# Performance work log

Hardware: AMD Instinct MI355X
Metric: run time of the kernel (lower is better)

The kernel has to match this reference:

```python
import jax, jax.numpy as jnp
import numpy as np

B, T, D, H, L, O = 256, 256, 512, 512, 3, 256
EPS = 1e-5


def setup_inputs() -> dict:
    key = jax.random.key(0)
    ks = jax.random.split(key, 8)
    rn = lambda i, shape, scale=1.0: jax.random.normal(ks[i], shape, dtype=jnp.float32) * scale
    z = lambda *shape: jnp.zeros(shape, jnp.float32)
    o = lambda *shape: jnp.ones(shape, jnp.float32)
    return {
        "x": rn(0, (B, T, D)),
        # layer 0 (non-middle) cell
        "W0": rn(1, (H, D), 0.02), "b0": z(H), "u0": rn(2, (H,)),
        "g1_0": o(H), "be1_0": z(H), "g2_0": o(H), "be2_0": z(H),
        # shared middle cell (layers 1..L-1 share one parameter set)
        "Wm": rn(3, (H, H), 0.02), "bm": z(H), "um": rn(4, (H,)),
        "g1_m": o(H), "be1_m": z(H), "g2_m": o(H), "be2_m": z(H),
        # output head
        "Wfc": rn(5, (O, H), 0.02), "bfc": z(O),
        "batchSize": B,
    }


def _bn(zx, g, b):
    # BatchNorm1d, training mode: batch stats over axis 0, biased variance
    m = jnp.mean(zx, axis=0)
    v = jnp.mean((zx - m) ** 2, axis=0)
    return (zx - m) * jax.lax.rsqrt(v + EPS) * g + b


def _cell(inp, h, W, bb, u, g1, be1, g2, be2):
    out = _bn(inp @ W.T + bb, g1, be1)
    out = jax.nn.relu(out + h * u)  # u is diagonal -> elementwise scale
    return _bn(out, g2, be2)


def reference(x, W0, b0, u0, g1_0, be1_0, g2_0, be2_0,
              Wm, bm, um, g1_m, be1_m, g2_m, be2_m, Wfc, bfc, batchSize):
    nmid = L - 1

    def step(carry, x_t):
        h0, hm = carry  # h0: [B,H], hm: [L-1,B,H]
        h0n = _cell(x_t, h0, W0, b0, u0, g1_0, be1_0, g2_0, be2_0)
        cur = h0n
        new = []
        for j in range(nmid):  # middle layers share params, distinct states
            hj = _cell(cur, hm[j], Wm, bm, um, g1_m, be1_m, g2_m, be2_m)
            new.append(hj)
            cur = hj
        return (h0n, jnp.stack(new)), None

    init = (jnp.zeros((batchSize, H), x.dtype),
            jnp.zeros((nmid, batchSize, H), x.dtype))
    (h0f, hmf), _ = jax.lax.scan(step, init, jnp.swapaxes(x, 0, 1))
    logits = hmf[-1] @ Wfc.T + bfc
    return jax.nn.log_softmax(logits, axis=-1)
```

## Files before the change

### kernel.cpp

```cpp
#include <hip/hip_runtime.h>
#include <math.h>

#define kT 256
#define kEPS 1e-5f
#define NBB 96
#define BT 1024
#define SSTEP 8
#define NT (kT / SSTEP)

typedef __attribute__((ext_vector_type(8))) _Float16 half8;
typedef __attribute__((ext_vector_type(4))) float f32x4;

#define BSLOT(p, j) (((p)*4 + (j)) * 16)
#define BARBYTES (260 * 4 * 64)

__device__ __forceinline__ unsigned packhl(float f) {
    _Float16 hi = (_Float16)f;
    _Float16 lo = (_Float16)(f - (float)hi);
    unsigned short uh, ul;
    __builtin_memcpy(&uh, &hi, 2);
    __builtin_memcpy(&ul, &lo, 2);
    return (unsigned)uh | ((unsigned)ul << 16);
}

__device__ __forceinline__ float unpackhl(unsigned wd) {
    unsigned short uh = (unsigned short)wd, ul = (unsigned short)(wd >> 16);
    _Float16 hi, lo;
    __builtin_memcpy(&hi, &uh, 2);
    __builtin_memcpy(&lo, &ul, 2);
    return (float)hi + (float)lo;
}

__device__ __forceinline__ void split32(uint4 A, uint4 B, half8& hi, half8& lo) {
    unsigned hh[4], ll[4];
    hh[0] = __builtin_amdgcn_perm(A.y, A.x, 0x05040100u);
    ll[0] = __builtin_amdgcn_perm(A.y, A.x, 0x07060302u);
    hh[1] = __builtin_amdgcn_perm(A.w, A.z, 0x05040100u);
    ll[1] = __builtin_amdgcn_perm(A.w, A.z, 0x07060302u);
    hh[2] = __builtin_amdgcn_perm(B.y, B.x, 0x05040100u);
    ll[2] = __builtin_amdgcn_perm(B.y, B.x, 0x07060302u);
    hh[3] = __builtin_amdgcn_perm(B.w, B.z, 0x05040100u);
    ll[3] = __builtin_amdgcn_perm(B.w, B.z, 0x07060302u);
    __builtin_memcpy(&hi, hh, 16);
    __builtin_memcpy(&lo, ll, 16);
}

__global__ __launch_bounds__(256) void w0pack(const float* __restrict__ W0,
                                              unsigned* __restrict__ W0p) {
    const int i4 = (blockIdx.x * 256 + threadIdx.x) * 4;
    float4 v = *(const float4*)(W0 + i4);
    uint4 pw;
    pw.x = packhl(v.x); pw.y = packhl(v.y); pw.z = packhl(v.z); pw.w = packhl(v.w);
    *(uint4*)(W0p + i4) = pw;
}

#define ZROWS 32
#define XSTR 516
__global__ __launch_bounds__(1024, 4) void zgemm(float* __restrict__ x,
                                                 const unsigned* __restrict__ W0p) {
    __shared__ unsigned xs[ZROWS * XSTR];
    const int tid = threadIdx.x;
    const long long r0 = (long long)blockIdx.x * ZROWS;

    {
        const int row = tid >> 5;
        const int k0 = (tid & 31) * 16;
        const float* src = x + (r0 + row) * 512 + k0;
        unsigned* dst = xs + row * XSTR + k0;
#pragma unroll
        for (int i = 0; i < 4; ++i) {
            float4 v = *(const float4*)(src + i * 4);
            uint4 pw;
            pw.x = packhl(v.x); pw.y = packhl(v.y); pw.z = packhl(v.z); pw.w = packhl(v.w);
            *(uint4*)(dst + i * 4) = pw;
        }
    }
    __syncthreads();

    const int w = tid >> 6, lane = tid & 63, q = lane >> 4, c = lane & 15;
    const int mt0 = w * 2;
    f32x4 acc[2][2] = {};
#pragma unroll
    for (int ks = 0; ks < 16; ++ks) {
        half8 ahi[2], alo[2], bhi[2], blo[2];
#pragma unroll
        for (int m = 0; m < 2; ++m) {
            const unsigned* ap = W0p + ((mt0 + m) * 16 + c) * 512 + ks * 32 + q * 8;
            split32(*(const uint4*)ap, *(const uint4*)(ap + 4), ahi[m], alo[m]);
        }
#pragma unroll
        for (int s = 0; s < 2; ++s) {
            const unsigned* bp = xs + (s * 16 + c) * XSTR + ks * 32 + q * 8;
            split32(*(const uint4*)bp, *(const uint4*)(bp + 4), bhi[s], blo[s]);
        }
#pragma unroll
        for (int m = 0; m < 2; ++m)
#pragma unroll
            for (int s = 0; s < 2; ++s) {
                acc[m][s] = __builtin_amdgcn_mfma_f32_16x16x32_f16(ahi[m], bhi[s], acc[m][s], 0, 0, 0);
                acc[m][s] = __builtin_amdgcn_mfma_f32_16x16x32_f16(ahi[m], blo[s], acc[m][s], 0, 0, 0);
                acc[m][s] = __builtin_amdgcn_mfma_f32_16x16x32_f16(alo[m], bhi[s], acc[m][s], 0, 0, 0);
            }
    }
    unsigned* zw = (unsigned*)x;
#pragma unroll
    for (int m = 0; m < 2; ++m)
#pragma unroll
        for (int s = 0; s < 2; ++s) {
            unsigned* zp = zw + (r0 + s * 16 + c) * 512 + (mt0 + m) * 16 + q * 4;
            uint4 pw;
            pw.x = packhl(acc[m][s][0]); pw.y = packhl(acc[m][s][1]);
            pw.z = packhl(acc[m][s][2]); pw.w = packhl(acc[m][s][3]);
            *(uint4*)zp = pw;
        }
}

__device__ __forceinline__ void grid_barrier(int* bar, int phase) {
    __syncthreads();
    if (threadIdx.x == 0) {
        const int slot = blockIdx.x & 3;
        __hip_atomic_fetch_add(&bar[BSLOT(phase, slot)], 1, __ATOMIC_RELAXED, __HIP_MEMORY_SCOPE_AGENT);
        int s;
        do {
            s = 0;
#pragma unroll
            for (int j = 0; j < 4; ++j)
                s += __hip_atomic_load(&bar[BSLOT(phase, j)], __ATOMIC_RELAXED, __HIP_MEMORY_SCOPE_AGENT);
            if (s < NBB) __builtin_amdgcn_s_sleep(2);
        } while (s < NBB);
    }
    __syncthreads();
    __builtin_amdgcn_fence(__ATOMIC_ACQUIRE, "agent");
}

__device__ __forceinline__ void bn_stats1(const f32x4 v, float* bnS, float* bnQ,
                                          float* bnM, float* bnR, int q, int c, int w, int tid) {
    float s[4], sq[4];
#pragma unroll
    for (int r = 0; r < 4; ++r) { s[r] = v[r]; sq[r] = v[r] * v[r]; }
#pragma unroll
    for (int mk = 1; mk < 16; mk <<= 1) {
#pragma unroll
        for (int r = 0; r < 4; ++r) {
            s[r]  += __shfl_xor(s[r],  mk, 64);
            sq[r] += __shfl_xor(sq[r], mk, 64);
        }
    }
    if (c == 0) {
#pragma unroll
        for (int r = 0; r < 4; ++r) { bnS[(q*4+r)*16 + w] = s[r]; bnQ[(q*4+r)*16 + w] = sq[r]; }
    }
    __syncthreads();
    if (tid < 16) {
        const float4* pS = (const float4*)(bnS + tid * 16);
        const float4* pQ = (const float4*)(bnQ + tid * 16);
        float4 s0 = pS[0], s1 = pS[1], s2 = pS[2], s3 = pS[3];
        float4 q0 = pQ[0], q1 = pQ[1], q2 = pQ[2], q3 = pQ[3];
        float S = (s0.x + s0.y + s0.z + s0.w) + (s1.x + s1.y + s1.z + s1.w)
                + (s2.x + s2.y + s2.z + s2.w) + (s3.x + s3.y + s3.z + s3.w);
        float Q = (q0.x + q0.y + q0.z + q0.w) + (q1.x + q1.y + q1.z + q1.w)
                + (q2.x + q2.y + q2.z + q2.w) + (q3.x + q3.y + q3.z + q3.w);
        float mn  = S * (1.f/256.f);
        float var = Q * (1.f/256.f) - mn * mn;
        bnM[tid] = mn; bnR[tid] = rsqrtf(var + kEPS);
    }
    __syncthreads();
}

__device__ __forceinline__ void bn_tail1(const f32x4 acc, f32x4& h, const float* pp,
                                         float* bnS, float* bnQ, float* bnM, float* bnR,
                                         int q, int c, int w, int tid) {
    bn_stats1(acc, bnS, bnQ, bnM, bnR, q, c, w, tid);
    f32x4 tmp;
#pragma unroll
    for (int r = 0; r < 4; ++r) {
        int m = q*4 + r;
        float zn = (acc[r] - bnM[m]) * bnR[m] * pp[16+m] + pp[32+m];
        float rl = zn + h[r] * pp[m];
        tmp[r] = rl > 0.f ? rl : 0.f;
    }
    bn_stats1(tmp, bnS, bnQ, bnM, bnR, q, c, w, tid);
#pragma unroll
    for (int r = 0; r < 4; ++r) {
        int m = q*4 + r;
        h[r] = (tmp[r] - bnM[m]) * bnR[m] * pp[48+m] + pp[64+m];
    }
}

#define PL64 32768

__device__ __forceinline__ void store_h1(unsigned* hp, const f32x4 h,
                                         int c0, int q, int c, int w) {
    unsigned long long* hpu = (unsigned long long*)hp;
    const int b = w*16 + c;
    const int g = (c0 >> 3) + (q >> 1);
    const long long idx = ((long long)g*256 + b)*2 + (q & 1);
    unsigned short uh[4], ul[4];
#pragma unroll
    for (int j = 0; j < 4; ++j) {
        _Float16 hi = (_Float16)h[j];
        _Float16 lo = (_Float16)(h[j] - (float)hi);
        __builtin_memcpy(&uh[j], &hi, 2);
        __builtin_memcpy(&ul[j], &lo, 2);
    }
    unsigned long long H, L;
    __builtin_memcpy(&H, uh, 8);
    __builtin_memcpy(&L, ul, 8);
    __hip_atomic_store(hpu + idx,        H, __ATOMIC_RELAXED, __HIP_MEMORY_SCOPE_AGENT);
    __hip_atomic_store(hpu + idx + PL64, L, __ATOMIC_RELAXED, __HIP_MEMORY_SCOPE_AGENT);
}

__device__ __forceinline__ void cell_h1(const unsigned* __restrict__ hw,
                                        const unsigned short* waHi, const unsigned short* waLo,
                                        f32x4& h, const float* pp,
                                        float* bnS, float* bnQ, float* bnM, float* bnR,
                                        unsigned* hpdst, int c0, int q, int c, int w, int tid) {
    f32x4 acc = {};
    const uint4* ph = (const uint4*)hw + (q*256 + w*16 + c);
    const uint4* pl = ph + 16384;
    uint4 Bh[8], Bl[8];
#pragma unroll
    for (int i = 0; i < 8; ++i) {
        Bh[i] = ph[i*1024];
        Bl[i] = pl[i*1024];
    }
#pragma unroll
    for (int i = 0; i < 8; ++i) {
        half8 bhi, blo;
        __builtin_memcpy(&bhi, &Bh[i], 16);
        __builtin_memcpy(&blo, &Bl[i], 16);
        half8 ahi = *(const half8*)(waHi + i*512);
        half8 alo = *(const half8*)(waLo + i*512);
        acc = __builtin_amdgcn_mfma_f32_16x16x32_f16(ahi, bhi, acc, 0, 0, 0);
        acc = __builtin_amdgcn_mfma_f32_16x16x32_f16(ahi, blo, acc, 0, 0, 0);
        acc = __builtin_amdgcn_mfma_f32_16x16x32_f16(alo, bhi, acc, 0, 0, 0);
        Bh[i] = ph[(i + 8)*1024];
        Bl[i] = pl[(i + 8)*1024];
    }
#pragma unroll
    for (int i = 0; i < 8; ++i) {
        half8 bhi, blo;
        __builtin_memcpy(&bhi, &Bh[i], 16);
        __builtin_memcpy(&blo, &Bl[i], 16);
        half8 ahi = *(const half8*)(waHi + (8 + i)*512);
        half8 alo = *(const half8*)(waLo + (8 + i)*512);
        acc = __builtin_amdgcn_mfma_f32_16x16x32_f16(ahi, bhi, acc, 0, 0, 0);
        acc = __builtin_amdgcn_mfma_f32_16x16x32_f16(ahi, blo, acc, 0, 0, 0);
        acc = __builtin_amdgcn_mfma_f32_16x16x32_f16(alo, bhi, acc, 0, 0, 0);
    }
    bn_tail1(acc, h, pp, bnS, bnQ, bnM, bnR, q, c, w, tid);
    if (hpdst) store_h1(hpdst, h, c0, q, c, w);
}

__device__ __forceinline__ void cell0lite(const unsigned* __restrict__ z0, int t,
                                          f32x4& h0, const float* pp,
                                          float* bnS, float* bnQ, float* bnM, float* bnR,
                                          unsigned* hpdst, int c0, int q, int c, int w, int tid) {
    const unsigned* zp = z0 + (long long)(w*16 + c)*131072LL + (long long)t*512 + c0 + q*4;
    uint4 zw = *(const uint4*)zp;
    f32x4 acc;
    acc[0] = unpackhl(zw.x); acc[1] = unpackhl(zw.y);
    acc[2] = unpackhl(zw.z); acc[3] = unpackhl(zw.w);
    bn_tail1(acc, h0, pp, bnS, bnQ, bnM, bnR, q, c, w, tid);
    store_h1(hpdst, h0, c0, q, c, w);
}

__global__ __launch_bounds__(BT, 4) void indrnn(
    const unsigned* __restrict__ z0,
    const float* __restrict__ Wm,
    const float* __restrict__ u0,  const float* __restrict__ g10,
    const float* __restrict__ be10, const float* __restrict__ g20,
    const float* __restrict__ be20,
    const float* __restrict__ um,  const float* __restrict__ g1m,
    const float* __restrict__ be1m, const float* __restrict__ g2m,
    const float* __restrict__ be2m,
    const float* __restrict__ Wfc, const float* __restrict__ bfc,
    float* __restrict__ out, int* __restrict__ bar,
    unsigned* __restrict__ hpws,
    float* __restrict__ h2n)
{
    __shared__ __align__(16) unsigned short WAhi_m[8192];
    __shared__ __align__(16) unsigned short WAlo_m[8192];
    __shared__ float bnS[256], bnQ[256], bnM[16], bnR[16];
    __shared__ float prm[160];

    const int tid  = threadIdx.x;
    const int blk  = blockIdx.x;
    const int role = blk >> 5;
    const int cid  = blk & 31;
    const int lane = tid & 63;
    const int w    = tid >> 6;
    const int q    = lane >> 4;
    const int c    = lane & 15;
    const int c0   = cid * 16;

    if (role != 0) {
        int e = tid;
        int ks = e >> 6, l = e & 63;
        int cc = l & 15, qq = l >> 4;
        const float* sm = Wm + (size_t)(c0 + cc)*512 + ks*32 + qq*8;
        unsigned short mh[8], ml[8];
#pragma unroll
        for (int j = 0; j < 8; ++j) {
            unsigned pm = packhl(sm[j]);
            mh[j] = (unsigned short)pm; ml[j] = (unsigned short)(pm >> 16);
        }
        __builtin_memcpy(&WAhi_m[e*8], mh, 16);
        __builtin_memcpy(&WAlo_m[e*8], ml, 16);
    }
    if (tid < 16) {
        prm[tid]      = u0[c0+tid];   prm[16+tid]  = g10[c0+tid];  prm[32+tid]  = be10[c0+tid];
        prm[48+tid]   = g20[c0+tid];  prm[64+tid]  = be20[c0+tid];
        prm[80+tid]   = um[c0+tid];   prm[96+tid]  = g1m[c0+tid];  prm[112+tid] = be1m[c0+tid];
        prm[128+tid]  = g2m[c0+tid];  prm[144+tid] = be2m[c0+tid];
    }
    __syncthreads();

    f32x4 h0 = {}, h1 = {}, h2 = {};
    const unsigned short* waHi = WAhi_m + lane*8;
    const unsigned short* waLo = WAlo_m + lane*8;
    unsigned* E0 = hpws;
    unsigned* E1 = hpws + SSTEP*2*131072;

    for (int tau = 0; tau <= NT + 1; ++tau) {
        if (role == 0) {
            if (tau < NT) {
                const int p = tau & 1;
                for (int i = 0; i < SSTEP; ++i)
                    cell0lite(z0, tau*SSTEP + i, h0, prm, bnS, bnQ, bnM, bnR,
                              E0 + (p*SSTEP + i)*131072, c0, q, c, w, tid);
            }
        } else if (role == 1) {
            if (tau >= 1 && tau <= NT) {
                const int p = (tau - 1) & 1;
                for (int i = 0; i < SSTEP; ++i)
                    cell_h1(E0 + (p*SSTEP + i)*131072, waHi, waLo, h1, prm + 80,
                            bnS, bnQ, bnM, bnR, E1 + (p*SSTEP + i)*131072,
                            c0, q, c, w, tid);
            }
        } else {
            if (tau >= 2) {
                const int p = tau & 1;
                for (int i = 0; i < SSTEP; ++i)
                    cell_h1(E1 + (p*SSTEP + i)*131072, waHi, waLo, h2, prm + 80,
                            bnS, bnQ, bnM, bnR, (unsigned*)nullptr, c0, q, c, w, tid);
            }
        }
        grid_barrier(bar, tau);
    }

    if (role == 2) {
        unsigned long long* h2u = (unsigned long long*)h2n;
        const int b = w*16 + c;
#pragma unroll
        for (int pr = 0; pr < 2; ++pr) {
            float fv[2] = { h2[pr*2], h2[pr*2+1] };
            unsigned long long val;
            __builtin_memcpy(&val, fv, 8);
            __hip_atomic_store(h2u + (((size_t)b*512 + c0 + q*4) >> 1) + pr, val,
                               __ATOMIC_RELAXED, __HIP_MEMORY_SCOPE_AGENT);
        }
    }
    grid_barrier(bar, NT + 2);

    if (blk < 32) {
        float* hs = (float*)WAhi_m;
        __syncthreads();
        ((float4*)hs)[tid] = ((const float4*)(h2n + (size_t)blk*4096))[tid];
        __syncthreads();
        if (w < 8) {
            const int row = w;
            const int o0  = lane * 4;
            const float* hrow = hs + row*512;
            float dots[4] = {bfc[o0], bfc[o0+1], bfc[o0+2], bfc[o0+3]};
#pragma unroll 4
            for (int h = 0; h < 512; h += 4) {
                float4 hv = *(const float4*)(hrow + h);
#pragma unroll
                for (int oo = 0; oo < 4; ++oo) {
                    float4 wv = *(const float4*)(Wfc + (size_t)(o0+oo)*512 + h);
                    dots[oo] += hv.x*wv.x + hv.y*wv.y + hv.z*wv.z + hv.w*wv.w;
                }
            }
            float M = fmaxf(fmaxf(dots[0], dots[1]), fmaxf(dots[2], dots[3]));
#pragma unroll
            for (int mk = 1; mk < 64; mk <<= 1) M = fmaxf(M, __shfl_xor(M, mk, 64));
            float S = 0.f;
#pragma unroll
            for (int oo = 0; oo < 4; ++oo) S += expf(dots[oo] - M);
#pragma unroll
            for (int mk = 1; mk < 64; mk <<= 1) S += __shfl_xor(S, mk, 64);
            float lse = M + logf(S);
#pragma unroll
            for (int oo = 0; oo < 4; ++oo)
                out[(size_t)(blk*8 + row)*256 + o0 + oo] = dots[oo] - lse;
        }
    }
}

extern "C" void kernel_launch(void* const* d_in, const int* in_sizes, int n_in,
                              void* d_out, int out_size, void* d_ws, size_t ws_size,
                              hipStream_t stream) {
    float* x          = (float*)d_in[0];
    const float* W0   = (const float*)d_in[1];
    const float* u0   = (const float*)d_in[3];
    const float* g10  = (const float*)d_in[4];
    const float* be10 = (const float*)d_in[5];
    const float* g20  = (const float*)d_in[6];
    const float* be20 = (const float*)d_in[7];
    const float* Wm   = (const float*)d_in[8];
    const float* um   = (const float*)d_in[10];
    const float* g1m  = (const float*)d_in[11];
    const float* be1m = (const float*)d_in[12];
    const float* g2m  = (const float*)d_in[13];
    const float* be2m = (const float*)d_in[14];
    const float* Wfc  = (const float*)d_in[15];
    const float* bfc  = (const float*)d_in[16];
    float* out = (float*)d_out;

    char* ws = (char*)d_ws;
    int* bar        = (int*)ws;
    unsigned* hpws  = (unsigned*)(ws + 131072);
    float* h2n      = (float*)(ws + 131072 + 16777216);
    unsigned* W0p   = (unsigned*)(ws + 131072 + 17301504);

    hipMemsetAsync(bar, 0, BARBYTES, stream);
    hipLaunchKernelGGL(w0pack, dim3(256), dim3(256), 0, stream, W0, W0p);
    hipLaunchKernelGGL(zgemm, dim3(2048), dim3(1024), 0, stream, x, W0p);
    hipLaunchKernelGGL(indrnn, dim3(NBB), dim3(BT), 0, stream,
                       (const unsigned*)x, Wm, u0, g10, be10, g20, be20,
                       um, g1m, be1m, g2m, be2m, Wfc, bfc,
                       out, bar, hpws, h2n);
}
```

Measured before the change: 3.141 ms.

## Batch GEMMs for all substeps before serial BN tails in each stage

Splits the per-timestep cell into a GEMM part and a batchnorm/recurrence tail. Within each superstep, all SSTEP input projections (z0 loads for layer 0, MFMA GEMMs for middle layers) are issued first, then the serial BN tails run. The GEMM inputs do not depend on the recurrent state, so their latency can overlap instead of alternating with the barrier-heavy BN reductions. This raises register pressure (8 accumulators held live, unrolled loops) under launch bounds of 1024 threads, which risks spills.

```diff
diff --git a/kernel.cpp b/kernel.cpp
--- a/kernel.cpp
+++ b/kernel.cpp
@@ -210,11 +210,10 @@
     __hip_atomic_store(hpu + idx + PL64, L, __ATOMIC_RELAXED, __HIP_MEMORY_SCOPE_AGENT);
 }
 
-__device__ __forceinline__ void cell_h1(const unsigned* __restrict__ hw,
-                                        const unsigned short* waHi, const unsigned short* waLo,
-                                        f32x4& h, const float* pp,
-                                        float* bnS, float* bnQ, float* bnM, float* bnR,
-                                        unsigned* hpdst, int c0, int q, int c, int w, int tid) {
+__device__ __forceinline__ f32x4 cell_gemm(const unsigned* __restrict__ hw,
+                                           const unsigned short* waHi,
+                                           const unsigned short* waLo,
+                                           int q, int c, int w) {
     f32x4 acc = {};
     const uint4* ph = (const uint4*)hw + (q*256 + w*16 + c);
     const uint4* pl = ph + 16384;
@@ -248,21 +247,7 @@
         acc = __builtin_amdgcn_mfma_f32_16x16x32_f16(ahi, blo, acc, 0, 0, 0);
         acc = __builtin_amdgcn_mfma_f32_16x16x32_f16(alo, bhi, acc, 0, 0, 0);
     }
-    bn_tail1(acc, h, pp, bnS, bnQ, bnM, bnR, q, c, w, tid);
-    if (hpdst) store_h1(hpdst, h, c0, q, c, w);
-}
-
-__device__ __forceinline__ void cell0lite(const unsigned* __restrict__ z0, int t,
-                                          f32x4& h0, const float* pp,
-                                          float* bnS, float* bnQ, float* bnM, float* bnR,
-                                          unsigned* hpdst, int c0, int q, int c, int w, int tid) {
-    const unsigned* zp = z0 + (long long)(w*16 + c)*131072LL + (long long)t*512 + c0 + q*4;
-    uint4 zw = *(const uint4*)zp;
-    f32x4 acc;
-    acc[0] = unpackhl(zw.x); acc[1] = unpackhl(zw.y);
-    acc[2] = unpackhl(zw.z); acc[3] = unpackhl(zw.w);
-    bn_tail1(acc, h0, pp, bnS, bnQ, bnM, bnR, q, c, w, tid);
-    store_h1(hpdst, h0, c0, q, c, w);
+    return acc;
 }
 
 __global__ __launch_bounds__(BT, 4) void indrnn(
@@ -326,24 +311,45 @@
         if (role == 0) {
             if (tau < NT) {
                 const int p = tau & 1;
-                for (int i = 0; i < SSTEP; ++i)
-                    cell0lite(z0, tau*SSTEP + i, h0, prm, bnS, bnQ, bnM, bnR,
-                              E0 + (p*SSTEP + i)*131072, c0, q, c, w, tid);
+                f32x4 acc[SSTEP];
+#pragma unroll
+                for (int i = 0; i < SSTEP; ++i) {
+                    const int t = tau*SSTEP + i;
+                    const unsigned* zp = z0 + (long long)(w*16 + c)*131072LL
+                                       + (long long)t*512 + c0 + q*4;
+                    uint4 zw = *(const uint4*)zp;
+                    acc[i][0] = unpackhl(zw.x); acc[i][1] = unpackhl(zw.y);
+                    acc[i][2] = unpackhl(zw.z); acc[i][3] = unpackhl(zw.w);
+                }
+#pragma unroll
+                for (int i = 0; i < SSTEP; ++i) {
+                    bn_tail1(acc[i], h0, prm, bnS, bnQ, bnM, bnR, q, c, w, tid);
+                    store_h1(E0 + (p*SSTEP + i)*131072, h0, c0, q, c, w);
+                }
             }
         } else if (role == 1) {
             if (tau >= 1 && tau <= NT) {
                 const int p = (tau - 1) & 1;
+                f32x4 acc[SSTEP];
+#pragma unroll
                 for (int i = 0; i < SSTEP; ++i)
-                    cell_h1(E0 + (p*SSTEP + i)*131072, waHi, waLo, h1, prm + 80,
-                            bnS, bnQ, bnM, bnR, E1 + (p*SSTEP + i)*131072,
-                            c0, q, c, w, tid);
+                    acc[i] = cell_gemm(E0 + (p*SSTEP + i)*131072, waHi, waLo, q, c, w);
+#pragma unroll
+                for (int i = 0; i < SSTEP; ++i) {
+                    bn_tail1(acc[i], h1, prm + 80, bnS, bnQ, bnM, bnR, q, c, w, tid);
+                    store_h1(E1 + (p*SSTEP + i)*131072, h1, c0, q, c, w);
+                }
             }
         } else {
             if (tau >= 2) {
                 const int p = tau & 1;
+                f32x4 acc[SSTEP];
+#pragma unroll
                 for (int i = 0; i < SSTEP; ++i)
-                    cell_h1(E1 + (p*SSTEP + i)*131072, waHi, waLo, h2, prm + 80,
-                            bnS, bnQ, bnM, bnR, (unsigned*)nullptr, c0, q, c, w, tid);
+                    acc[i] = cell_gemm(E1 + (p*SSTEP + i)*131072, waHi, waLo, q, c, w);
+#pragma unroll
+                for (int i = 0; i < SSTEP; ++i)
+                    bn_tail1(acc[i], h2, prm + 80, bnS, bnQ, bnM, bnR, q, c, w, tid);
             }
         }
         grid_barrier(bar, tau);
```

Result: slower. 3.624 ms (+15.4%).
